# Kernel tuning notes

Measured on AMD Instinct MI355X. Metric: run time of the kernel, lower is better.

The kernel has to match this reference:

```python
import jax, jax.numpy as jnp
import numpy as np

WH, WW = 8, 8
DIM, HEADS = 512, 16
HEAD_DIM = DIM // HEADS
SCALE = HEAD_DIM ** (-0.5)


def _rel_pos_index(wh, ww):
    # Swin relative position index, computed once with numpy (static).
    coords = np.stack(np.meshgrid(np.arange(wh), np.arange(ww), indexing='ij'))  # [2,wh,ww]
    cf = coords.reshape(2, -1)                                # [2, N]
    rel = cf[:, :, None] - cf[:, None, :]                     # [2, N, N]
    rel = rel.transpose(1, 2, 0).astype(np.int64)             # [N, N, 2]
    rel[..., 0] += wh - 1
    rel[..., 1] += ww - 1
    rel[..., 0] *= 2 * ww - 1
    return jnp.asarray(rel.sum(-1))                           # [N, N]

REL_IDX = _rel_pos_index(WH, WW)


def setup_inputs() -> dict:
    key = jax.random.key(0)
    ks = jax.random.split(key, 12)
    B_, N, C = 1024, WH * WW, DIM
    nW = 64
    std = C ** (-0.5)
    return {
        'q': jax.random.normal(ks[0], (B_, N, C), jnp.float32),
        'k': jax.random.normal(ks[1], (B_, N, C), jnp.float32),
        'v': jax.random.normal(ks[2], (B_, N, C), jnp.float32),
        'mask': jnp.zeros((nW, N, N), jnp.float32),
        'Wq': jax.random.normal(ks[3], (C, C), jnp.float32) * std,
        'bq': jnp.zeros((C,), jnp.float32),
        'Wk': jax.random.normal(ks[4], (C, C), jnp.float32) * std,
        'bk': jnp.zeros((C,), jnp.float32),
        'Wv': jax.random.normal(ks[5], (C, C), jnp.float32) * std,
        'bv': jnp.zeros((C,), jnp.float32),
        'Wp': jax.random.normal(ks[6], (C, C), jnp.float32) * std,
        'bp': jnp.zeros((C,), jnp.float32),
        'bias_table': jax.random.normal(ks[7], ((2 * WH - 1) * (2 * WW - 1), HEADS), jnp.float32) * 0.02,
    }


def reference(q, k, v, mask, Wq, bq, Wk, bk, Wv, bv, Wp, bp, bias_table):
    B_, N, C = q.shape
    H, hd = HEADS, HEAD_DIM

    def heads(x, W, b):  # Linear then split heads -> [B_, H, N, hd]
        return (x @ W.T + b).reshape(B_, N, H, hd).transpose(0, 2, 1, 3)

    qh = heads(q, Wq, bq) * SCALE
    kh = heads(k, Wk, bk)
    vh = heads(v, Wv, bv)

    attn = jnp.einsum('bhnd,bhmd->bhnm', qh, kh)              # [B_, H, N, N]
    rel_bias = bias_table[REL_IDX.reshape(-1)].reshape(N, N, H).transpose(2, 0, 1)  # [H,N,N]
    attn = attn + rel_bias[None]

    nW = mask.shape[0]
    attn = attn.reshape(B_ // nW, nW, H, N, N) + mask[None, :, None]
    attn = attn.reshape(B_, H, N, N)
    attn = jax.nn.softmax(attn, axis=-1)

    x = jnp.einsum('bhnm,bhmd->bhnd', attn, vh)
    x = x.transpose(0, 2, 1, 3).reshape(B_, N, C)
    return x @ Wp.T + bp
```

## Files before the change

kernel.cpp:

```cpp
#include <hip/hip_runtime.h>
#include <hip/hip_bf16.h>

typedef __attribute__((ext_vector_type(4))) float  f32x4;
typedef __attribute__((ext_vector_type(8))) short  bf16x8;
typedef __attribute__((ext_vector_type(4))) short  short4_t;
typedef unsigned short u16;

#define SCALE_Q 0.17677669529663687f

__device__ __forceinline__ u16 f2bf(float f) {
    union { float f; unsigned u; } v; v.f = f;
    unsigned u = v.u;
    return (u16)((u + 0x7FFFu + ((u >> 16) & 1u)) >> 16);
}

__device__ __forceinline__ void load_lds16(const void* g, void* l) {
    __builtin_amdgcn_global_load_lds(
        (const __attribute__((address_space(1))) void*)g,
        (__attribute__((address_space(3))) void*)l, 16, 0, 0);
}

__global__ __launch_bounds__(256) void cvt_kernel(
        const float* __restrict__ s, u16* __restrict__ d, int n8)
{
    const int i = blockIdx.x * 256 + threadIdx.x;
    if (i >= n8) return;
    const float4* sp = (const float4*)s + (size_t)i * 2;
    const float4 a = sp[0], b = sp[1];
    bf16x8 o;
    o[0] = (short)f2bf(a.x); o[1] = (short)f2bf(a.y);
    o[2] = (short)f2bf(a.z); o[3] = (short)f2bf(a.w);
    o[4] = (short)f2bf(b.x); o[5] = (short)f2bf(b.y);
    o[6] = (short)f2bf(b.z); o[7] = (short)f2bf(b.w);
    *((bf16x8*)d + i) = o;
}

__global__ __launch_bounds__(256) void cwb_kernel(
        const float* __restrict__ bias_table,
        const float* __restrict__ mask,
        float* __restrict__ cwb)
{
    const int wh = blockIdx.x;
    const int w = wh >> 4, h = wh & 15;
    for (int e = threadIdx.x; e < 4096; e += 256) {
        const int i = e >> 6, j = e & 63;
        const int rel = ((i >> 3) - (j >> 3) + 7) * 15 + (i & 7) - (j & 7) + 7;
        cwb[(size_t)wh * 4096 + e] = bias_table[rel * 16 + h] + mask[(size_t)w * 4096 + e];
    }
}

template<int OMODE>
__global__ __launch_bounds__(256) void gemm_bf16(
        const u16* __restrict__ A, const u16* __restrict__ Wb,
        const float* __restrict__ bias, float scale, void* __restrict__ outp)
{
    __shared__ __align__(16) u16 As[8192];
    __shared__ __align__(16) u16 Bs[8192];

    const int t  = threadIdx.x;
    const int m0 = blockIdx.y << 7;
    const int n0 = blockIdx.x << 7;
    const int lane = t & 63, wv = t >> 6;
    const int g = lane >> 4, ln = lane & 15;
    const int wr = wv >> 1, wc = wv & 1;
    const int wbase = wv << 6;

    f32x4 acc[4][4];
#pragma unroll
    for (int i = 0; i < 4; i++)
#pragma unroll
        for (int j = 0; j < 4; j++) acc[i][j] = {0.f, 0.f, 0.f, 0.f};

    const u16* Abase = A  + (size_t)m0 * 512;
    const u16* Bbase = Wb + (size_t)n0 * 512;

    for (int k0 = 0; k0 < 512; k0 += 64) {
#pragma unroll
        for (int c = 0; c < 4; c++) {
            const int bi  = (c << 8) + wbase + lane;
            const int row = bi >> 3;
            const int cbs = (bi & 7) ^ (row & 7);
            const size_t go = (size_t)row * 512 + k0 + (cbs << 3);
            u16* ldst = (c & 1) ? &Bs[(((c >> 1) << 9) + (wbase << 1)) << 3]
                                : &As[(((c >> 1) << 9) + (wbase << 1)) << 3];
            (void)ldst;
            load_lds16(Abase + go, &As[((c << 8) + wbase) << 3]);
            load_lds16(Bbase + go, &Bs[((c << 8) + wbase) << 3]);
        }
        __syncthreads();
#pragma unroll
        for (int ks = 0; ks < 2; ks++) {
            bf16x8 af[4], bfr[4];
#pragma unroll
            for (int mt = 0; mt < 4; mt++) {
                const int row = (wr << 6) + (mt << 4) + ln;
                af[mt] = *(const bf16x8*)&As[(row << 6) + ((((ks << 2) + g) ^ (row & 7)) << 3)];
            }
#pragma unroll
            for (int nt = 0; nt < 4; nt++) {
                const int row = (wc << 6) + (nt << 4) + ln;
                bfr[nt] = *(const bf16x8*)&Bs[(row << 6) + ((((ks << 2) + g) ^ (row & 7)) << 3)];
            }
#pragma unroll
            for (int mt = 0; mt < 4; mt++)
#pragma unroll
                for (int nt = 0; nt < 4; nt++)
                    acc[mt][nt] = __builtin_amdgcn_mfma_f32_16x16x32_bf16(
                        af[mt], bfr[nt], acc[mt][nt], 0, 0, 0);
        }
        __syncthreads();
    }

#pragma unroll
    for (int mt = 0; mt < 4; mt++) {
#pragma unroll
        for (int nt = 0; nt < 4; nt++) {
            const int n = n0 + (wc << 6) + (nt << 4) + ln;
            const float bv = bias[n];
            const int mbase = m0 + (wr << 6) + (mt << 4) + (g << 2);
            if (OMODE == 0) {
#pragma unroll
                for (int r = 0; r < 4; r++) {
                    const int m = mbase + r;
                    const int b = m >> 6, tt = m & 63, hh = n >> 5, d = n & 31;
                    ((u16*)outp)[((size_t)(b * 16 + hh) * 64 + tt) * 32 + d] =
                        f2bf((acc[mt][nt][r] + bv) * scale);
                }
            } else if (OMODE == 1) {
                short4_t hq;
#pragma unroll
                for (int r = 0; r < 4; r++) hq[r] = (short)f2bf((acc[mt][nt][r] + bv) * scale);
                const int b = mbase >> 6, tt = mbase & 63, hh = n >> 5, d = n & 31;
                *(short4_t*)&((u16*)outp)[((size_t)(b * 16 + hh) * 32 + d) * 64 + tt] = hq;
            } else {
#pragma unroll
                for (int r = 0; r < 4; r++) {
                    const int m = mbase + r;
                    ((float*)outp)[(size_t)m * 512 + n] = (acc[mt][nt][r] + bv) * scale;
                }
            }
        }
    }
}

__global__ __launch_bounds__(64) void attn_kernel(
        const u16* __restrict__ qh, const u16* __restrict__ kh,
        const u16* __restrict__ vt, const float* __restrict__ cwb,
        u16* __restrict__ xout)
{
    __shared__ __align__(16) u16 P[4096];

    const int bid = blockIdx.x;
    const int b = bid >> 4, h = bid & 15, w = b & 63;
    const int lane = threadIdx.x, g = lane >> 4, ln = lane & 15;
    const size_t base = (size_t)bid * 2048;

    bf16x8 kf[4], qf[4];
#pragma unroll
    for (int mt = 0; mt < 4; mt++)
        kf[mt] = *(const bf16x8*)&kh[base + (mt * 16 + ln) * 32 + g * 8];
#pragma unroll
    for (int nt = 0; nt < 4; nt++)
        qf[nt] = *(const bf16x8*)&qh[base + (nt * 16 + ln) * 32 + g * 8];

    f32x4 acc[4][4];
#pragma unroll
    for (int i = 0; i < 4; i++)
#pragma unroll
        for (int j = 0; j < 4; j++) acc[i][j] = {0.f, 0.f, 0.f, 0.f};

#pragma unroll
    for (int mt = 0; mt < 4; mt++)
#pragma unroll
        for (int nt = 0; nt < 4; nt++)
            acc[mt][nt] = __builtin_amdgcn_mfma_f32_16x16x32_bf16(
                kf[mt], qf[nt], acc[mt][nt], 0, 0, 0);

    const float* cw = cwb + (size_t)(w * 16 + h) * 4096;
#pragma unroll
    for (int nt = 0; nt < 4; nt++) {
        const int i = nt * 16 + ln;
#pragma unroll
        for (int mt = 0; mt < 4; mt++) {
            const float4 bm = *(const float4*)&cw[i * 64 + mt * 16 + (g << 2)];
            acc[mt][nt][0] += bm.x; acc[mt][nt][1] += bm.y;
            acc[mt][nt][2] += bm.z; acc[mt][nt][3] += bm.w;
        }
    }

#pragma unroll
    for (int nt = 0; nt < 4; nt++) {
        float mx = acc[0][nt][0];
#pragma unroll
        for (int mt = 0; mt < 4; mt++)
#pragma unroll
            for (int r = 0; r < 4; r++) mx = fmaxf(mx, acc[mt][nt][r]);
        mx = fmaxf(mx, __shfl_xor(mx, 16));
        mx = fmaxf(mx, __shfl_xor(mx, 32));
        float sum = 0.f;
#pragma unroll
        for (int mt = 0; mt < 4; mt++)
#pragma unroll
            for (int r = 0; r < 4; r++) {
                const float p = __expf(acc[mt][nt][r] - mx);
                acc[mt][nt][r] = p;
                sum += p;
            }
        sum += __shfl_xor(sum, 16);
        sum += __shfl_xor(sum, 32);
        const float rs = 1.0f / sum;
        const int i = nt * 16 + ln;
#pragma unroll
        for (int mt = 0; mt < 4; mt++) {
            short4_t hq;
#pragma unroll
            for (int r = 0; r < 4; r++) hq[r] = (short)f2bf(acc[mt][nt][r] * rs);
            const int idx = (i * 64 + mt * 16 + (g << 2)) ^ ((i & 7) << 3);
            *(short4_t*)&P[idx] = hq;
        }
    }
    __syncthreads();

    f32x4 oacc[2][4];
#pragma unroll
    for (int i = 0; i < 2; i++)
#pragma unroll
        for (int j = 0; j < 4; j++) oacc[i][j] = {0.f, 0.f, 0.f, 0.f};

#pragma unroll
    for (int ks = 0; ks < 2; ks++) {
        bf16x8 vf[2], pf[4];
#pragma unroll
        for (int mt = 0; mt < 2; mt++)
            vf[mt] = *(const bf16x8*)&vt[base + (mt * 16 + ln) * 64 + ks * 32 + g * 8];
#pragma unroll
        for (int nt = 0; nt < 4; nt++) {
            const int i = nt * 16 + ln;
            pf[nt] = *(const bf16x8*)&P[(i * 64 + ks * 32 + g * 8) ^ ((i & 7) << 3)];
        }
#pragma unroll
        for (int mt = 0; mt < 2; mt++)
#pragma unroll
            for (int nt = 0; nt < 4; nt++)
                oacc[mt][nt] = __builtin_amdgcn_mfma_f32_16x16x32_bf16(
                    vf[mt], pf[nt], oacc[mt][nt], 0, 0, 0);
    }

#pragma unroll
    for (int mt = 0; mt < 2; mt++) {
#pragma unroll
        for (int nt = 0; nt < 4; nt++) {
            const int i = nt * 16 + ln, d0 = mt * 16 + (g << 2);
            short4_t hq;
#pragma unroll
            for (int r = 0; r < 4; r++) hq[r] = (short)f2bf(oacc[mt][nt][r]);
            *(short4_t*)&xout[((size_t)b * 64 + i) * 512 + h * 32 + d0] = hq;
        }
    }
}

extern "C" void kernel_launch(void* const* d_in, const int* in_sizes, int n_in,
                              void* d_out, int out_size, void* d_ws, size_t ws_size,
                              hipStream_t stream) {
    const float* q    = (const float*)d_in[0];
    const float* k    = (const float*)d_in[1];
    const float* v    = (const float*)d_in[2];
    const float* mask = (const float*)d_in[3];
    const float* Wq   = (const float*)d_in[4];
    const float* bq   = (const float*)d_in[5];
    const float* Wk   = (const float*)d_in[6];
    const float* bk   = (const float*)d_in[7];
    const float* Wv   = (const float*)d_in[8];
    const float* bv   = (const float*)d_in[9];
    const float* Wp   = (const float*)d_in[10];
    const float* bp   = (const float*)d_in[11];
    const float* bias_table = (const float*)d_in[12];
    float* out = (float*)d_out;

    char* ws = (char*)d_ws;
    u16*   t0  = (u16*)(ws);
    u16*   qh  = (u16*)(ws + 67108864);
    u16*   kh  = (u16*)(ws + 134217728);
    u16*   vt  = (u16*)(ws + 201326592);
    float* cwb = (float*)(ws + 268435456);
    u16*   wqb = (u16*)(ws + 285212672);
    u16*   wkb = (u16*)(ws + 285736960);
    u16*   wvb = (u16*)(ws + 286261248);
    u16*   wpb = (u16*)(ws + 286785536);

    const int n8_act = (1024 * 64 * 512) / 8;
    const int n8_w   = (512 * 512) / 8;

    cwb_kernel<<<1024, 256, 0, stream>>>(bias_table, mask, cwb);
    cvt_kernel<<<n8_w / 256, 256, 0, stream>>>(Wq, wqb, n8_w);
    cvt_kernel<<<n8_w / 256, 256, 0, stream>>>(Wk, wkb, n8_w);
    cvt_kernel<<<n8_w / 256, 256, 0, stream>>>(Wv, wvb, n8_w);
    cvt_kernel<<<n8_w / 256, 256, 0, stream>>>(Wp, wpb, n8_w);

    cvt_kernel<<<n8_act / 256, 256, 0, stream>>>(q, t0, n8_act);
    gemm_bf16<0><<<dim3(4, 512), 256, 0, stream>>>(t0, wqb, bq, SCALE_Q, (void*)qh);

    cvt_kernel<<<n8_act / 256, 256, 0, stream>>>(k, t0, n8_act);
    gemm_bf16<0><<<dim3(4, 512), 256, 0, stream>>>(t0, wkb, bk, 1.0f, (void*)kh);

    cvt_kernel<<<n8_act / 256, 256, 0, stream>>>(v, t0, n8_act);
    gemm_bf16<1><<<dim3(4, 512), 256, 0, stream>>>(t0, wvb, bv, 1.0f, (void*)vt);

    attn_kernel<<<16384, 64, 0, stream>>>(qh, kh, vt, cwb, t0);

    gemm_bf16<2><<<dim3(4, 512), 256, 0, stream>>>(t0, wpb, bp, 1.0f, (void*)out);
}
```

Before: 459.2 us.

## Pack four attention heads per block, remap GEMM blocks, merge weight converts

The attention kernel now runs four independent head-windows per 256-thread block, each wave using its own LDS slice, instead of one 64-thread block per head. GEMM blocks are launched on a 1D grid and remapped so that consecutive blocks land on different XCDs while sharing A rows. The four weight-conversion launches are merged into one, and the manual bf16 rounding is replaced with the compiler's native __bf16 cast. Together these aim to cut launch count, improve occupancy and L2 locality, and shorten conversion code, at the cost of a block-wide barrier now coupling four waves in attention.

Result: faster. 429.1 us (-6.6%).

```diff
diff --git a/kernel.cpp b/kernel.cpp
--- a/kernel.cpp
+++ b/kernel.cpp
@@ -8,10 +8,9 @@
 
 #define SCALE_Q 0.17677669529663687f
 
-__device__ __forceinline__ u16 f2bf(float f) {
-    union { float f; unsigned u; } v; v.f = f;
-    unsigned u = v.u;
-    return (u16)((u + 0x7FFFu + ((u >> 16) & 1u)) >> 16);
+__device__ __forceinline__ short bfc(float f) {
+    __bf16 b = (__bf16)f;
+    union { __bf16 b; short s; } u; u.b = b; return u.s;
 }
 
 __device__ __forceinline__ void load_lds16(const void* g, void* l) {
@@ -28,10 +27,27 @@
     const float4* sp = (const float4*)s + (size_t)i * 2;
     const float4 a = sp[0], b = sp[1];
     bf16x8 o;
-    o[0] = (short)f2bf(a.x); o[1] = (short)f2bf(a.y);
-    o[2] = (short)f2bf(a.z); o[3] = (short)f2bf(a.w);
-    o[4] = (short)f2bf(b.x); o[5] = (short)f2bf(b.y);
-    o[6] = (short)f2bf(b.z); o[7] = (short)f2bf(b.w);
+    o[0] = bfc(a.x); o[1] = bfc(a.y); o[2] = bfc(a.z); o[3] = bfc(a.w);
+    o[4] = bfc(b.x); o[5] = bfc(b.y); o[6] = bfc(b.z); o[7] = bfc(b.w);
+    *((bf16x8*)d + i) = o;
+}
+
+__global__ __launch_bounds__(256) void wcvt_kernel(
+        const float* __restrict__ w0, const float* __restrict__ w1,
+        const float* __restrict__ w2, const float* __restrict__ w3,
+        u16* __restrict__ d0, u16* __restrict__ d1,
+        u16* __restrict__ d2, u16* __restrict__ d3)
+{
+    const float* s = (blockIdx.y == 0) ? w0 : (blockIdx.y == 1) ? w1
+                   : (blockIdx.y == 2) ? w2 : w3;
+    u16* d = (blockIdx.y == 0) ? d0 : (blockIdx.y == 1) ? d1
+           : (blockIdx.y == 2) ? d2 : d3;
+    const int i = blockIdx.x * 256 + threadIdx.x;
+    const float4* sp = (const float4*)s + (size_t)i * 2;
+    const float4 a = sp[0], b = sp[1];
+    bf16x8 o;
+    o[0] = bfc(a.x); o[1] = bfc(a.y); o[2] = bfc(a.z); o[3] = bfc(a.w);
+    o[4] = bfc(b.x); o[5] = bfc(b.y); o[6] = bfc(b.z); o[7] = bfc(b.w);
     *((bf16x8*)d + i) = o;
 }
 
@@ -50,16 +66,18 @@
 }
 
 template<int OMODE>
-__global__ __launch_bounds__(256) void gemm_bf16(
+__global__ __launch_bounds__(256) void gemm_b(
         const u16* __restrict__ A, const u16* __restrict__ Wb,
         const float* __restrict__ bias, float scale, void* __restrict__ outp)
 {
     __shared__ __align__(16) u16 As[8192];
     __shared__ __align__(16) u16 Bs[8192];
 
-    const int t  = threadIdx.x;
-    const int m0 = blockIdx.y << 7;
-    const int n0 = blockIdx.x << 7;
+    const int wg = (blockIdx.x & 7) * 256 + (blockIdx.x >> 3);
+    const int m0 = (wg >> 2) << 7;
+    const int n0 = (wg & 3) << 7;
+
+    const int t = threadIdx.x;
     const int lane = t & 63, wv = t >> 6;
     const int g = lane >> 4, ln = lane & 15;
     const int wr = wv >> 1, wc = wv & 1;
@@ -81,9 +99,6 @@
             const int row = bi >> 3;
             const int cbs = (bi & 7) ^ (row & 7);
             const size_t go = (size_t)row * 512 + k0 + (cbs << 3);
-            u16* ldst = (c & 1) ? &Bs[(((c >> 1) << 9) + (wbase << 1)) << 3]
-                                : &As[(((c >> 1) << 9) + (wbase << 1)) << 3];
-            (void)ldst;
             load_lds16(Abase + go, &As[((c << 8) + wbase) << 3]);
             load_lds16(Bbase + go, &Bs[((c << 8) + wbase) << 3]);
         }
@@ -124,12 +139,12 @@
                     const int m = mbase + r;
                     const int b = m >> 6, tt = m & 63, hh = n >> 5, d = n & 31;
                     ((u16*)outp)[((size_t)(b * 16 + hh) * 64 + tt) * 32 + d] =
-                        f2bf((acc[mt][nt][r] + bv) * scale);
+                        (u16)bfc((acc[mt][nt][r] + bv) * scale);
                 }
             } else if (OMODE == 1) {
                 short4_t hq;
 #pragma unroll
-                for (int r = 0; r < 4; r++) hq[r] = (short)f2bf((acc[mt][nt][r] + bv) * scale);
+                for (int r = 0; r < 4; r++) hq[r] = bfc((acc[mt][nt][r] + bv) * scale);
                 const int b = mbase >> 6, tt = mbase & 63, hh = n >> 5, d = n & 31;
                 *(short4_t*)&((u16*)outp)[((size_t)(b * 16 + hh) * 32 + d) * 64 + tt] = hq;
             } else {
@@ -143,17 +158,19 @@
     }
 }
 
-__global__ __launch_bounds__(64) void attn_kernel(
+__global__ __launch_bounds__(256) void attn_kernel(
         const u16* __restrict__ qh, const u16* __restrict__ kh,
         const u16* __restrict__ vt, const float* __restrict__ cwb,
         u16* __restrict__ xout)
 {
-    __shared__ __align__(16) u16 P[4096];
-
-    const int bid = blockIdx.x;
+    __shared__ __align__(16) u16 P[16384];
+
+    const int wv = threadIdx.x >> 6;
+    const int bid = (blockIdx.x << 2) + wv;
     const int b = bid >> 4, h = bid & 15, w = b & 63;
-    const int lane = threadIdx.x, g = lane >> 4, ln = lane & 15;
+    const int lane = threadIdx.x & 63, g = lane >> 4, ln = lane & 15;
     const size_t base = (size_t)bid * 2048;
+    u16* Pw = &P[wv << 12];
 
     bf16x8 kf[4], qf[4];
 #pragma unroll
@@ -214,9 +231,9 @@
         for (int mt = 0; mt < 4; mt++) {
             short4_t hq;
 #pragma unroll
-            for (int r = 0; r < 4; r++) hq[r] = (short)f2bf(acc[mt][nt][r] * rs);
+            for (int r = 0; r < 4; r++) hq[r] = bfc(acc[mt][nt][r] * rs);
             const int idx = (i * 64 + mt * 16 + (g << 2)) ^ ((i & 7) << 3);
-            *(short4_t*)&P[idx] = hq;
+            *(short4_t*)&Pw[idx] = hq;
         }
     }
     __syncthreads();
@@ -236,7 +253,7 @@
 #pragma unroll
         for (int nt = 0; nt < 4; nt++) {
             const int i = nt * 16 + ln;
-            pf[nt] = *(const bf16x8*)&P[(i * 64 + ks * 32 + g * 8) ^ ((i & 7) << 3)];
+            pf[nt] = *(const bf16x8*)&Pw[(i * 64 + ks * 32 + g * 8) ^ ((i & 7) << 3)];
         }
 #pragma unroll
         for (int mt = 0; mt < 2; mt++)
@@ -253,7 +270,7 @@
             const int i = nt * 16 + ln, d0 = mt * 16 + (g << 2);
             short4_t hq;
 #pragma unroll
-            for (int r = 0; r < 4; r++) hq[r] = (short)f2bf(oacc[mt][nt][r]);
+            for (int r = 0; r < 4; r++) hq[r] = bfc(oacc[mt][nt][r]);
             *(short4_t*)&xout[((size_t)b * 64 + i) * 512 + h * 32 + d0] = hq;
         }
     }
@@ -289,24 +306,20 @@
     u16*   wpb = (u16*)(ws + 286785536);
 
     const int n8_act = (1024 * 64 * 512) / 8;
-    const int n8_w   = (512 * 512) / 8;
 
     cwb_kernel<<<1024, 256, 0, stream>>>(bias_table, mask, cwb);
-    cvt_kernel<<<n8_w / 256, 256, 0, stream>>>(Wq, wqb, n8_w);
-    cvt_kernel<<<n8_w / 256, 256, 0, stream>>>(Wk, wkb, n8_w);
-    cvt_kernel<<<n8_w / 256, 256, 0, stream>>>(Wv, wvb, n8_w);
-    cvt_kernel<<<n8_w / 256, 256, 0, stream>>>(Wp, wpb, n8_w);
+    wcvt_kernel<<<dim3(128, 4), 256, 0, stream>>>(Wq, Wk, Wv, Wp, wqb, wkb, wvb, wpb);
 
     cvt_kernel<<<n8_act / 256, 256, 0, stream>>>(q, t0, n8_act);
-    gemm_bf16<0><<<dim3(4, 512), 256, 0, stream>>>(t0, wqb, bq, SCALE_Q, (void*)qh);
+    gemm_b<0><<<2048, 256, 0, stream>>>(t0, wqb, bq, SCALE_Q, (void*)qh);
 
     cvt_kernel<<<n8_act / 256, 256, 0, stream>>>(k, t0, n8_act);
-    gemm_bf16<0><<<dim3(4, 512), 256, 0, stream>>>(t0, wkb, bk, 1.0f, (void*)kh);
+    gemm_b<0><<<2048, 256, 0, stream>>>(t0, wkb, bk, 1.0f, (void*)kh);
 
     cvt_kernel<<<n8_act / 256, 256, 0, stream>>>(v, t0, n8_act);
-    gemm_bf16<1><<<dim3(4, 512), 256, 0, stream>>>(t0, wvb, bv, 1.0f, (void*)vt);
-
-    attn_kernel<<<16384, 64, 0, stream>>>(qh, kh, vt, cwb, t0);
-
-    gemm_bf16<2><<<dim3(4, 512), 256, 0, stream>>>(t0, wpb, bp, 1.0f, (void*)out);
-}
+    gemm_b<1><<<2048, 256, 0, stream>>>(t0, wvb, bv, 1.0f, (void*)vt);
+
+    attn_kernel<<<4096, 256, 0, stream>>>(qh, kh, vt, cwb, t0);
+
+    gemm_b<2><<<2048, 256, 0, stream>>>(t0, wpb, bp, 1.0f, (void*)out);
+}
```
